# Kernel optimization log

Measured on AMD Instinct MI355X. Metric: run time of the kernel, lower is better.

Reference implementation:

```python
import jax, jax.numpy as jnp
import numpy as np

L, B, P, D, H, DH, KV, M, S, A = 12, 8, 800, 1024, 8, 256, 1, 4096, 50, 32
ROPE_BASE = 10000.0
NEG = -1e30


def _rms(x, w):
    return (x * jax.lax.rsqrt(jnp.mean(x * x, -1, keepdims=True) + 1e-6)) * (1.0 + w)


def _rope(x, cos, sin):
    # x: [B,h,S,DH]; cos/sin: [B,1,S,DH//2]
    x1, x2 = jnp.split(x, 2, axis=-1)
    return jnp.concatenate([x1 * cos - x2 * sin, x2 * cos + x1 * sin], -1)


def setup_inputs() -> dict:
    key = jax.random.key(0)
    ks = iter(jax.random.split(key, 40))
    def nrm(shape, s=0.02):
        return jax.random.normal(next(ks), shape, jnp.float32) * s
    return {
        'prefix_pad_masks': jnp.ones((B, P), jnp.bool_),
        'x_t': jax.random.normal(next(ks), (B, S, A), jnp.float32),
        'timestep': jax.random.uniform(next(ks), (B,), jnp.float32),
        'dt': jnp.full((1,), 0.1, jnp.float32),
        'cache_k': nrm((L, B, KV, P, DH), 1.0),
        'cache_v': nrm((L, B, KV, P, DH), 1.0),
        'w_act_in': nrm((A, D)), 'b_act_in': jnp.zeros((D,), jnp.float32),
        'w_t1': nrm((D, D)), 'b_t1': jnp.zeros((D,), jnp.float32),
        'w_t2': nrm((D, D)), 'b_t2': jnp.zeros((D,), jnp.float32),
        'ln1_w': jnp.zeros((L, D), jnp.float32),
        'ada1_w': nrm((L, D, D)),
        'ln2_w': jnp.zeros((L, D), jnp.float32),
        'wq': nrm((L, D, H * DH)), 'wk': nrm((L, D, KV * DH)),
        'wv': nrm((L, D, KV * DH)), 'wo': nrm((L, H * DH, D)),
        'wg': nrm((L, D, M)), 'wu': nrm((L, D, M)), 'wd': nrm((L, M, D)),
        'lnf_w': jnp.zeros((D,), jnp.float32), 'adaf_w': nrm((D, D)),
        'w_act_out': nrm((D, A)), 'b_act_out': jnp.zeros((A,), jnp.float32),
    }


def reference(prefix_pad_masks, x_t, timestep, dt, cache_k, cache_v,
              w_act_in, b_act_in, w_t1, b_t1, w_t2, b_t2,
              ln1_w, ada1_w, ln2_w, wq, wk, wv, wo, wg, wu, wd,
              lnf_w, adaf_w, w_act_out, b_act_out):
    b, s, _ = x_t.shape
    p = prefix_pad_masks.shape[1]
    # --- embed_suffix: action projection + sinusoidal time -> MLP -> adaRMS cond ---
    suffix = x_t @ w_act_in + b_act_in                              # [B,S,D]
    half = D // 2
    freqs = jnp.exp(-jnp.log(jnp.float32(10000.0)) * jnp.arange(half, dtype=jnp.float32) / half)
    ang = timestep[:, None] * freqs[None, :]
    temb = jnp.concatenate([jnp.sin(ang), jnp.cos(ang)], -1)        # [B,D]
    cond = jax.nn.silu(temb @ w_t1 + b_t1) @ w_t2 + b_t2            # adarms_cond [B,D]
    # --- prefix-suffix 2D attention mask (make_att_2d_masks_trt) ---
    suffix_pad = jnp.ones((b, s), jnp.int32)
    suffix_att = jnp.concatenate([jnp.ones((b, 1), jnp.int32), jnp.zeros((b, s - 1), jnp.int32)], 1)
    cums = jnp.cumsum(suffix_att, 1)
    att2d = cums[:, None, :] <= cums[:, :, None]
    pad2d = (suffix_pad[:, None, :] * suffix_pad[:, :, None]).astype(bool)
    pre2d = jnp.broadcast_to(prefix_pad_masks[:, None, :], (b, s, p))
    full = jnp.concatenate([pre2d, att2d & pad2d], 2)               # [B,S,P+S]
    bias = jnp.where(full, 0.0, NEG)[:, None, :, :].astype(jnp.float32)
    # --- position ids: prefix offset + suffix cumsum - 1 ---
    offs = jnp.sum(prefix_pad_masks.astype(jnp.int32), -1)[:, None]
    pos = offs + jnp.cumsum(suffix_pad, 1) - 1                      # [B,S]
    inv = 1.0 / (ROPE_BASE ** (jnp.arange(0, DH, 2, dtype=jnp.float32) / DH))
    rang = pos[..., None].astype(jnp.float32) * inv                 # [B,S,DH/2]
    cos = jnp.cos(rang)[:, None]
    sin = jnp.sin(rang)[:, None]
    # --- gemma expert (eager attention over KV cache + suffix) ---
    h = suffix * jnp.sqrt(jnp.float32(D))
    def layer(hc, xs):
        l1, a1, l2, Wq, Wk, Wv, Wo, Wg, Wu, Wd, ck, cv = xs
        x = _rms(hc, l1) * (1.0 + (cond @ a1)[:, None, :])
        q = (x @ Wq).reshape(b, s, H, DH).transpose(0, 2, 1, 3)
        k = (x @ Wk).reshape(b, s, KV, DH).transpose(0, 2, 1, 3)
        v = (x @ Wv).reshape(b, s, KV, DH).transpose(0, 2, 1, 3)
        q = _rope(q, cos, sin)
        k = _rope(k, cos, sin)
        kf = jnp.repeat(jnp.concatenate([ck, k], 2), H // KV, 1)    # [B,H,P+S,DH]
        vf = jnp.repeat(jnp.concatenate([cv, v], 2), H // KV, 1)
        sc = jnp.einsum('bhsd,bhtd->bhst', q, kf) / jnp.sqrt(jnp.float32(DH)) + bias
        at = jax.nn.softmax(sc, -1)
        o = jnp.einsum('bhst,bhtd->bhsd', at, vf).transpose(0, 2, 1, 3).reshape(b, s, H * DH)
        hc = hc + o @ Wo
        x2 = _rms(hc, l2)
        hc = hc + (jax.nn.gelu(x2 @ Wg, approximate=True) * (x2 @ Wu)) @ Wd
        return hc, None
    h, _ = jax.lax.scan(layer, h, (ln1_w, ada1_w, ln2_w, wq, wk, wv, wo, wg, wu, wd, cache_k, cache_v))
    hf = _rms(h, lnf_w) * (1.0 + (cond @ adaf_w)[:, None, :])
    v_t = hf[:, -S:].astype(jnp.float32) @ w_act_out + b_act_out    # action_out_proj
    return x_t + dt.reshape(1, 1, 1) * v_t                          # Euler step
```

## Files before the change

### kernel.cpp

```cpp
#include <hip/hip_runtime.h>
#include <hip/hip_bf16.h>
#include <math.h>

#define NLAYER 12
#define NB 8
#define NP 800
#define ND 1024
#define NH 8
#define NDH 256
#define NM 4096
#define NS 50
#define NA 32
#define NKEYS 850
#define KPAD 1024

typedef unsigned short ushort_t;
typedef unsigned int u32;
using f32x4  = __attribute__((ext_vector_type(4))) float;
using short8 = __attribute__((ext_vector_type(8))) short;

__device__ __forceinline__ u32 pack_bf2(float lo, float hi) {
  u32 a = __float_as_uint(lo);
  u32 b = __float_as_uint(hi);
  a += 0x7fffu + ((a >> 16) & 1u);
  b += 0x7fffu + ((b >> 16) & 1u);
  return (a >> 16) | (b & 0xffff0000u);
}
__device__ __forceinline__ ushort_t bf1(float x) {
  u32 a = __float_as_uint(x);
  a += 0x7fffu + ((a >> 16) & 1u);
  return (ushort_t)(a >> 16);
}
__device__ __forceinline__ float ubf(ushort_t h) {
  return __uint_as_float(((u32)h) << 16);
}
__device__ __forceinline__ void async_cp16(const void* g, const void* l) {
  __builtin_amdgcn_global_load_lds(
      (const __attribute__((address_space(1))) u32*)g,
      (__attribute__((address_space(3))) u32*)l, 16, 0, 0);
}
#define SWZ(row, c) ((c) ^ (((row) & 7) << 3))


__global__ void cvt_permute_kernel(const float* __restrict__ src, ushort_t* __restrict__ dst, long nrows) {
  long idx = (long)blockIdx.x * 256 + threadIdx.x;
  long row = idx >> 5;
  int t = (int)(idx & 31);
  if (row >= nrows) return;
  const float* s = src + row * 256 + t * 4;
  float4 lo = *reinterpret_cast<const float4*>(s);
  float4 hi = *reinterpret_cast<const float4*>(s + 128);
  ushort_t* d = dst + row * 256 + t * 8;
  *reinterpret_cast<uint4*>(d) =
      make_uint4(pack_bf2(lo.x, hi.x), pack_bf2(lo.y, hi.y),
                 pack_bf2(lo.z, hi.z), pack_bf2(lo.w, hi.w));
}

template<int MODE>
__global__ __launch_bounds__(256) void transpose_cvt(
    const float* __restrict__ src, long sz, ushort_t* __restrict__ dst, long dz,
    int R, int C, int ldd, int halfOff) {
  __shared__ float Ls[64][65];
  const float* s = src + (long)blockIdx.z * sz;
  ushort_t* d    = dst + (long)blockIdx.z * dz;
  int c0 = blockIdx.x * 64, r0 = blockIdx.y * 64;
  int t = threadIdx.x;
  int rr = t >> 4;
  int cc = (t & 15) * 4;
#pragma unroll
  for (int j = 0; j < 4; ++j) {
    int rl = rr + j * 16;
    int r = r0 + rl;
    float4 v = make_float4(0.f, 0.f, 0.f, 0.f);
    if (r < R) v = *reinterpret_cast<const float4*>(s + (long)r * C + c0 + cc);
    Ls[rl][cc] = v.x; Ls[rl][cc+1] = v.y; Ls[rl][cc+2] = v.z; Ls[rl][cc+3] = v.w;
  }
  __syncthreads();
  int dr = t >> 2;
  int rc = (t & 3) * 16;
  int cg = c0 + dr;
  long orow;
  if (MODE == 0)      orow = cg;
  else if (MODE == 1) orow = ((long)(cg >> 5) << 6) + (cg & 31) + halfOff;
  else                orow = (long)(cg & ~255) + ((cg & 127) << 1) + ((cg >> 7) & 1);
  ushort_t* drow = d + orow * ldd + r0 + rc;
#pragma unroll
  for (int i = 0; i < 16; i += 2) {
    int sr = r0 + rc + i;
    if (sr < R) {
      u32 p = pack_bf2(Ls[rc + i][dr], Ls[rc + i + 1][dr]);
      *reinterpret_cast<u32*>(drow + i) = p;
    }
  }
}


__global__ void temb_kernel(const float* __restrict__ ts, float* __restrict__ temb) {
  int idx = blockIdx.x * 256 + threadIdx.x;
  if (idx >= NB * ND) return;
  int b = idx >> 10, d = idx & 1023;
  int i = d & 511;
  float f = __expf(-logf(10000.f) * (float)i / 512.f);
  float ang = ts[b] * f;
  temb[idx] = (d < 512) ? sinf(ang) : cosf(ang);
}

__global__ void suffix_kernel(const float* __restrict__ x_t, const float* __restrict__ w,
                              const float* __restrict__ bias, float* __restrict__ h) {
  int m = blockIdx.x;
  __shared__ float xs[NA];
  if (threadIdx.x < NA) xs[threadIdx.x] = x_t[m * NA + threadIdx.x];
  __syncthreads();
  for (int n = threadIdx.x; n < ND; n += 256) {
    float acc = bias[n];
#pragma unroll
    for (int k = 0; k < NA; ++k) acc += xs[k] * w[k * ND + n];
    h[m * ND + n] = acc * 32.0f;
  }
}

__global__ void rope_table_kernel(float* __restrict__ cosT, float* __restrict__ sinT) {
  int idx = blockIdx.x * 256 + threadIdx.x;
  if (idx >= NS * 128) return;
  int s = idx >> 7, i = idx & 127;
  float inv = __expf(-(float)(2 * i) / 256.f * logf(10000.f));
  float ang = (float)(NP + s) * inv;
  cosT[idx] = cosf(ang);
  sinT[idx] = sinf(ang);
}

template<bool BFOUT>
__global__ void rms_kernel(float* __restrict__ hin, const float* __restrict__ slabs,
                           const float* __restrict__ w,
                           const float* __restrict__ ada, void* __restrict__ outv) {
  int m = blockIdx.x;
  int b = m / NS;
  int d0 = threadIdx.x * 4;
  float4 v = *reinterpret_cast<const float4*>(hin + (long)m * ND + d0);
  if (slabs) {
#pragma unroll
    for (int c = 0; c < 4; ++c) {
      float4 sv = *reinterpret_cast<const float4*>(slabs + ((long)c * 400 + m) * ND + d0);
      v.x += sv.x; v.y += sv.y; v.z += sv.z; v.w += sv.w;
    }
    *reinterpret_cast<float4*>(hin + (long)m * ND + d0) = v;
  }
  float ss = v.x*v.x + v.y*v.y + v.z*v.z + v.w*v.w;
#pragma unroll
  for (int off = 32; off > 0; off >>= 1) ss += __shfl_down(ss, off);
  __shared__ float red[4];
  int lane = threadIdx.x & 63, wid = threadIdx.x >> 6;
  if (lane == 0) red[wid] = ss;
  __syncthreads();
  float tot = red[0] + red[1] + red[2] + red[3];
  float r = rsqrtf(tot * (1.f / ND) + 1e-6f);
  float4 wv = *reinterpret_cast<const float4*>(w + d0);
  float4 o;
  o.x = v.x * r * (1.f + wv.x);
  o.y = v.y * r * (1.f + wv.y);
  o.z = v.z * r * (1.f + wv.z);
  o.w = v.w * r * (1.f + wv.w);
  if (ada) {
    float4 av = *reinterpret_cast<const float4*>(ada + (long)b * ND + d0);
    o.x *= (1.f + av.x); o.y *= (1.f + av.y); o.z *= (1.f + av.z); o.w *= (1.f + av.w);
  }
  if (BFOUT) {
    *reinterpret_cast<uint2*>((ushort_t*)outv + (long)m * ND + d0) =
        make_uint2(pack_bf2(o.x, o.y), pack_bf2(o.z, o.w));
  } else {
    *reinterpret_cast<float4*>((float*)outv + (long)m * ND + d0) = o;
  }
}

__global__ void final_fused(const float* __restrict__ hin, const float* __restrict__ slabs,
                            const float* __restrict__ lnf,
                            const float* __restrict__ adaf, const float* __restrict__ w,
                            const float* __restrict__ bias, const float* __restrict__ x_t,
                            const float* __restrict__ dt, float* __restrict__ out) {
  int m = blockIdx.x;
  int b = m / NS;
  int d0 = threadIdx.x * 4;
  __shared__ float hfs[ND];
  __shared__ float red[256];
  float4 v = *reinterpret_cast<const float4*>(hin + (long)m * ND + d0);
#pragma unroll
  for (int c = 0; c < 4; ++c) {
    float4 sv = *reinterpret_cast<const float4*>(slabs + ((long)c * 400 + m) * ND + d0);
    v.x += sv.x; v.y += sv.y; v.z += sv.z; v.w += sv.w;
  }
  float ss = v.x*v.x + v.y*v.y + v.z*v.z + v.w*v.w;
#pragma unroll
  for (int off = 32; off > 0; off >>= 1) ss += __shfl_down(ss, off);
  __shared__ float red4[4];
  int lane = threadIdx.x & 63, wid = threadIdx.x >> 6;
  if (lane == 0) red4[wid] = ss;
  __syncthreads();
  float tot = red4[0] + red4[1] + red4[2] + red4[3];
  float r = rsqrtf(tot * (1.f / ND) + 1e-6f);
  float4 wv = *reinterpret_cast<const float4*>(lnf + d0);
  float4 av = *reinterpret_cast<const float4*>(adaf + (long)b * ND + d0);
  hfs[d0]     = v.x * r * (1.f + wv.x) * (1.f + av.x);
  hfs[d0 + 1] = v.y * r * (1.f + wv.y) * (1.f + av.y);
  hfs[d0 + 2] = v.z * r * (1.f + wv.z) * (1.f + av.z);
  hfs[d0 + 3] = v.w * r * (1.f + wv.w) * (1.f + av.w);
  __syncthreads();
  int a = threadIdx.x & 31;
  int kg = threadIdx.x >> 5;
  float acc = 0.f;
  for (int k = kg; k < ND; k += 8) acc += hfs[k] * w[k * NA + a];
  red[threadIdx.x] = acc;
  __syncthreads();
  if (threadIdx.x < NA) {
    float s = 0.f;
#pragma unroll
    for (int g = 0; g < 8; ++g) s += red[g * 32 + a];
    out[m * NA + a] = x_t[m * NA + a] + dt[0] * (s + bias[a]);
  }
}

__global__ __launch_bounds__(256) void gemm64slab(
    const ushort_t* __restrict__ A,
    const ushort_t* __restrict__ B,
    float* __restrict__ C,
    int M, int N, int K, int lda, int ldb, int ldc, int kpb) {
  const int flat3 = blockIdx.x + 7 * (blockIdx.y + 16 * blockIdx.z);
  const int wgid = (flat3 & 7) * 56 + (flat3 >> 3);
  const int chunk = wgid / 112;
  const int rem = wgid - chunk * 112;
  const int m0 = (rem % 7) * 64;
  const int n0 = (rem / 7) * 64;
  const int kbeg = chunk * kpb;
  const int kend = kbeg + kpb;

  const int tid = threadIdx.x;
  const int lane = tid & 63;
  const int wbase = tid & 192;
  const int wid = wbase >> 6;
  const int wm = (wid >> 1) * 32;
  const int wn = (wid & 1) * 32;
  const int l15 = lane & 15;
  const int l4  = lane >> 4;

  __shared__ ushort_t As[2][64 * 64];
  __shared__ ushort_t Bs[2][64 * 64];

  f32x4 acc[2][2] = {};

  const int ci0 = wbase + lane;
  const int row0 = ci0 >> 3;
  const int kc0 = (((ci0 & 7) ^ (row0 & 7)) << 3);
  const int ci1 = 256 + ci0;
  const int row1 = ci1 >> 3;
  const int kc1 = (((ci1 & 7) ^ (row1 & 7)) << 3);
  int gra0 = m0 + row0; if (gra0 > M - 1) gra0 = M - 1;
  int gra1 = m0 + row1; if (gra1 > M - 1) gra1 = M - 1;
  const int n_0 = n0 + row0;
  const int n_1 = n0 + row1;

  auto stage = [&](int buf, int k0) {
    async_cp16(A + (long)gra0 * lda + k0 + kc0, (const char*)As[buf] + ci0 * 16);
    async_cp16(B + (long)n_0 * ldb + k0 + kc0, (const char*)Bs[buf] + ci0 * 16);
    async_cp16(A + (long)gra1 * lda + k0 + kc1, (const char*)As[buf] + ci1 * 16);
    async_cp16(B + (long)n_1 * ldb + k0 + kc1, (const char*)Bs[buf] + ci1 * 16);
  };

  const int nt = (kend - kbeg) >> 6;
  stage(0, kbeg);
  __syncthreads();
  int cur = 0;
  for (int t = 0; t < nt; ++t) {
    if (t + 1 < nt) stage(cur ^ 1, kbeg + (t + 1) * 64);
    const ushort_t* Ac = As[cur];
    const ushort_t* Bc = Bs[cur];
#pragma unroll
    for (int ks = 0; ks < 2; ++ks) {
      short8 af[2], bf[2];
#pragma unroll
      for (int mi = 0; mi < 2; ++mi) {
        int row = wm + mi * 16 + l15;
        af[mi] = *reinterpret_cast<const short8*>(&Ac[row * 64 + SWZ(row, ks * 32 + l4 * 8)]);
      }
#pragma unroll
      for (int ni = 0; ni < 2; ++ni) {
        int row = wn + ni * 16 + l15;
        bf[ni] = *reinterpret_cast<const short8*>(&Bc[row * 64 + SWZ(row, ks * 32 + l4 * 8)]);
      }
#pragma unroll
      for (int mi = 0; mi < 2; ++mi)
#pragma unroll
        for (int ni = 0; ni < 2; ++ni)
          acc[mi][ni] = __builtin_amdgcn_mfma_f32_16x16x32_bf16(af[mi], bf[ni], acc[mi][ni], 0, 0, 0);
    }
    __syncthreads();
    cur ^= 1;
  }

  float* Cs = C + (long)chunk * 400 * ldc;
#pragma unroll
  for (int mi = 0; mi < 2; ++mi) {
#pragma unroll
    for (int ni = 0; ni < 2; ++ni) {
      int col = n0 + wn + ni * 16 + l15;
      int rb  = m0 + wm + mi * 16 + l4 * 4;
      if (col >= N) continue;
#pragma unroll
      for (int r = 0; r < 4; ++r) {
        int row = rb + r;
        if (row >= M) continue;
        Cs[(long)row * ldc + col] = acc[mi][ni][r];
      }
    }
  }
}

__global__ __launch_bounds__(256) void gemm64rope(
    const ushort_t* __restrict__ A,
    const ushort_t* __restrict__ B,
    const float* __restrict__ cosT, const float* __restrict__ sinT,
    ushort_t* __restrict__ qTo, ushort_t* __restrict__ k_new,
    ushort_t* __restrict__ vT_l) {
  const int M = 400, lda = 1024, ldb = 1024;
  const int flat = blockIdx.x + 7 * blockIdx.y;
  const int wgid = (flat & 7) * 35 + (flat >> 3);
  const int m0 = (wgid % 7) * 64;
  const int n0 = (wgid / 7) * 64;
  const int tid = threadIdx.x;
  const int lane = tid & 63;
  const int wbase = tid & 192;
  const int wid = wbase >> 6;
  const int wm = (wid >> 1) * 32;
  const int wn = (wid & 1) * 32;
  const int l15 = lane & 15;
  const int l4  = lane >> 4;

  __shared__ ushort_t As[2][64 * 64];
  __shared__ ushort_t Bs[2][64 * 64];

  f32x4 acc[2][2] = {};

  const int ci0 = wbase + lane;
  const int row0 = ci0 >> 3;
  const int kc0 = (((ci0 & 7) ^ (row0 & 7)) << 3);
  const int ci1 = 256 + ci0;
  const int row1 = ci1 >> 3;
  const int kc1 = (((ci1 & 7) ^ (row1 & 7)) << 3);
  int gra0 = m0 + row0; if (gra0 > M - 1) gra0 = M - 1;
  int gra1 = m0 + row1; if (gra1 > M - 1) gra1 = M - 1;
  const int n_0 = n0 + row0;
  const int n_1 = n0 + row1;

  auto stage = [&](int buf, int k0) {
    async_cp16(A + (long)gra0 * lda + k0 + kc0, (const char*)As[buf] + ci0 * 16);
    async_cp16(B + (long)n_0 * ldb + k0 + kc0, (const char*)Bs[buf] + ci0 * 16);
    async_cp16(A + (long)gra1 * lda + k0 + kc1, (const char*)As[buf] + ci1 * 16);
    async_cp16(B + (long)n_1 * ldb + k0 + kc1, (const char*)Bs[buf] + ci1 * 16);
  };

  stage(0, 0);
  __syncthreads();
  int cur = 0;
  for (int t = 0; t < 16; ++t) {
    if (t + 1 < 16) stage(cur ^ 1, (t + 1) * 64);
    const ushort_t* Ac = As[cur];
    const ushort_t* Bc = Bs[cur];
#pragma unroll
    for (int ks = 0; ks < 2; ++ks) {
      short8 af[2], bf[2];
#pragma unroll
      for (int mi = 0; mi < 2; ++mi) {
        int row = wm + mi * 16 + l15;
        af[mi] = *reinterpret_cast<const short8*>(&Ac[row * 64 + SWZ(row, ks * 32 + l4 * 8)]);
      }
#pragma unroll
      for (int ni = 0; ni < 2; ++ni) {
        int row = wn + ni * 16 + l15;
        bf[ni] = *reinterpret_cast<const short8*>(&Bc[row * 64 + SWZ(row, ks * 32 + l4 * 8)]);
      }
#pragma unroll
      for (int mi = 0; mi < 2; ++mi)
#pragma unroll
        for (int ni = 0; ni < 2; ++ni)
          acc[mi][ni] = __builtin_amdgcn_mfma_f32_16x16x32_bf16(af[mi], bf[ni], acc[mi][ni], 0, 0, 0);
    }
    __syncthreads();
    cur ^= 1;
  }

#pragma unroll
  for (int mi = 0; mi < 2; ++mi) {
#pragma unroll
    for (int ni = 0; ni < 2; ++ni) {
      int col = n0 + wn + ni * 16 + l15;
      int rb  = m0 + wm + mi * 16 + l4 * 4;
      float pv[4];
#pragma unroll
      for (int r = 0; r < 4; ++r) pv[r] = __shfl_xor(acc[mi][ni][r], 1);
#pragma unroll
      for (int r = 0; r < 4; ++r) {
        int row = rb + r;
        if (row >= 400) continue;
        int b = row / NS, s = row - b * NS;
        float v = acc[mi][ni][r];
        if (col < 2304) {
          int j = col & 255;
          int i = j >> 1;
          float c = cosT[s * 128 + i], sn = sinT[s * 128 + i];
          float o = (col & 1) ? (v * c + pv[r] * sn) : (v * c - pv[r] * sn);
          if (col < 2048)
            qTo[((long)((b << 3) + (col >> 8)) * NS + s) * 256 + j] = bf1(o);
          else
            k_new[(long)row * 256 + j] = bf1(o);
        } else {
          vT_l[((long)(b * 256 + (col - 2304))) * KPAD + NP + s] = bf1(v);
        }
      }
    }
  }
}

__global__ __launch_bounds__(256) void flash2_kernel(
    const ushort_t* __restrict__ qT,
    const ushort_t* __restrict__ kcache_l,
    const ushort_t* __restrict__ k_new,
    const ushort_t* __restrict__ vT_l,
    const ushort_t* __restrict__ zpad,
    float* __restrict__ opart, float* __restrict__ mpart, float* __restrict__ lpart) {
  const int flat = blockIdx.x + 64 * blockIdx.y;
  const int wgid = (flat & 7) * 32 + (flat >> 3);
  const int bh = wgid & 63;
  const int ch = wgid >> 6;
  const int b  = bh >> 3;
  const int tid = threadIdx.x;
  const int lane = tid & 63;
  const int w = tid >> 6;
  const int wm = (w >> 1) * 32;
  const int wn = (w & 1) * 128;
  const int l15 = lane & 15;
  const int l4  = lane >> 4;

  __shared__ __align__(16) char lds[100352];
  ushort_t* KV0 = (ushort_t*)lds;
  ushort_t* KV1 = (ushort_t*)(lds + 32768);
  ushort_t* Ps  = (ushort_t*)(lds + 65536);
  float* SMm = (float*)(lds + 99328);
  float* SMl = (float*)(lds + 99840);

  short8 qf[4][2][2];
  {
    const ushort_t* qbase = qT + (long)bh * NS * 256;
#pragma unroll
    for (int mi = 0; mi < 2; ++mi) {
      int row = wm + mi * 16 + l15;
      int qr = row < NS ? row : NS - 1;
      const ushort_t* qrow = qbase + (long)qr * 256;
#pragma unroll
      for (int s = 0; s < 4; ++s)
#pragma unroll
        for (int ks = 0; ks < 2; ++ks)
          qf[s][mi][ks] = *reinterpret_cast<const short8*>(qrow + s * 64 + ks * 32 + l4 * 8);
    }
  }

  auto stageK = [&](ushort_t* buf, int s) {
#pragma unroll
    for (int i = 0; i < 8; ++i) {
      int ci = i * 256 + tid;
      int key = ch * 256 + (ci >> 3);
      int seg = (ci ^ (ci >> 3)) & 7;
      const ushort_t* src;
      if (key < NP)         src = kcache_l + ((long)(b * NP + key)) * 256 + s * 64 + seg * 8;
      else if (key < NKEYS) src = k_new + ((long)(b * NS + key - NP)) * 256 + s * 64 + seg * 8;
      else                  src = zpad + seg * 8;
      async_cp16(src, (char*)buf + ci * 16);
    }
  };
  auto stageV = [&](ushort_t* buf, int s) {
#pragma unroll
    for (int i = 0; i < 8; ++i) {
      int ci = i * 256 + tid;
      int dout = ci >> 3;
      int seg = (ci ^ (ci >> 3)) & 7;
      async_cp16(vT_l + ((long)(b * 256 + dout)) * KPAD + ch * 256 + s * 64 + seg * 8,
                 (char*)buf + ci * 16);
    }
  };

  f32x4 s2[2][8] = {};
  stageK(KV0, 0);
  __syncthreads();
#pragma unroll
  for (int s = 0; s < 4; ++s) {
    ushort_t* buf = (s & 1) ? KV1 : KV0;
    ushort_t* nxt = (s & 1) ? KV0 : KV1;
    if (s < 3) stageK(nxt, s + 1);
    __builtin_amdgcn_s_setprio(1);
#pragma unroll
    for (int ks = 0; ks < 2; ++ks) {
      short8 bf[8];
#pragma unroll
      for (int ni = 0; ni < 8; ++ni) {
        int row = wn + ni * 16 + l15;
        bf[ni] = *reinterpret_cast<const short8*>(&buf[row * 64 + SWZ(row, ks * 32 + l4 * 8)]);
      }
#pragma unroll
      for (int mi = 0; mi < 2; ++mi)
#pragma unroll
        for (int ni = 0; ni < 8; ++ni)
          s2[mi][ni] = __builtin_amdgcn_mfma_f32_16x16x32_bf16(qf[s][mi][ks], bf[ni], s2[mi][ni], 0, 0, 0);
    }
    __builtin_amdgcn_s_setprio(0);
    __syncthreads();
  }

  stageV(KV0, 0);

  float mx[2][4];
#pragma unroll
  for (int mi = 0; mi < 2; ++mi)
#pragma unroll
    for (int r = 0; r < 4; ++r) mx[mi][r] = -1e30f;
#pragma unroll
  for (int mi = 0; mi < 2; ++mi)
#pragma unroll
    for (int ni = 0; ni < 8; ++ni) {
      int key = ch * 256 + wn + ni * 16 + l15;
      bool valid = key < NKEYS;
#pragma unroll
      for (int r = 0; r < 4; ++r) {
        float v = s2[mi][ni][r] * 0.0625f;
        v = valid ? v : -1e30f;
        s2[mi][ni][r] = v;
        mx[mi][r] = fmaxf(mx[mi][r], v);
      }
    }
#pragma unroll
  for (int off = 1; off < 16; off <<= 1)
#pragma unroll
    for (int mi = 0; mi < 2; ++mi)
#pragma unroll
      for (int r = 0; r < 4; ++r)
        mx[mi][r] = fmaxf(mx[mi][r], __shfl_xor(mx[mi][r], off));
  if (l15 == 0) {
#pragma unroll
    for (int mi = 0; mi < 2; ++mi)
#pragma unroll
      for (int r = 0; r < 4; ++r)
        SMm[(w & 1) * 64 + wm + mi * 16 + l4 * 4 + r] = mx[mi][r];
  }
  __syncthreads();
  float mrow[2][4], sum[2][4];
#pragma unroll
  for (int mi = 0; mi < 2; ++mi)
#pragma unroll
    for (int r = 0; r < 4; ++r) {
      int row = wm + mi * 16 + l4 * 4 + r;
      mrow[mi][r] = fmaxf(SMm[row], SMm[64 + row]);
      sum[mi][r] = 0.f;
    }
#pragma unroll
  for (int mi = 0; mi < 2; ++mi)
#pragma unroll
    for (int ni = 0; ni < 8; ++ni) {
      int colp = wn + ni * 16 + l15;
#pragma unroll
      for (int r = 0; r < 4; ++r) {
        float e = __expf(s2[mi][ni][r] - mrow[mi][r]);
        Ps[(wm + mi * 16 + l4 * 4 + r) * 264 + colp] = bf1(e);
        sum[mi][r] += e;
      }
    }
#pragma unroll
  for (int off = 1; off < 16; off <<= 1)
#pragma unroll
    for (int mi = 0; mi < 2; ++mi)
#pragma unroll
      for (int r = 0; r < 4; ++r)
        sum[mi][r] += __shfl_xor(sum[mi][r], off);
  if (l15 == 0) {
#pragma unroll
    for (int mi = 0; mi < 2; ++mi)
#pragma unroll
      for (int r = 0; r < 4; ++r)
        SMl[(w & 1) * 64 + wm + mi * 16 + l4 * 4 + r] = sum[mi][r];
  }
  __syncthreads();
  if ((w & 1) == 0 && l15 == 0) {
#pragma unroll
    for (int mi = 0; mi < 2; ++mi)
#pragma unroll
      for (int r = 0; r < 4; ++r) {
        int row = wm + mi * 16 + l4 * 4 + r;
        if (row < NS) {
          mpart[((long)bh * 4 + ch) * NS + row] = mrow[mi][r];
          lpart[((long)bh * 4 + ch) * NS + row] = SMl[row] + SMl[64 + row];
        }
      }
  }

  f32x4 o2[2][8] = {};
#pragma unroll
  for (int s = 0; s < 4; ++s) {
    ushort_t* buf = (s & 1) ? KV1 : KV0;
    ushort_t* nxt = (s & 1) ? KV0 : KV1;
    if (s < 3) stageV(nxt, s + 1);
    __builtin_amdgcn_s_setprio(1);
#pragma unroll
    for (int ks = 0; ks < 2; ++ks) {
      short8 af[2], bf[8];
#pragma unroll
      for (int mi = 0; mi < 2; ++mi)
        af[mi] = *reinterpret_cast<const short8*>(&Ps[(wm + mi * 16 + l15) * 264 + s * 64 + ks * 32 + l4 * 8]);
#pragma unroll
      for (int ni = 0; ni < 8; ++ni) {
        int row = wn + ni * 16 + l15;
        bf[ni] = *reinterpret_cast<const short8*>(&buf[row * 64 + SWZ(row, ks * 32 + l4 * 8)]);
      }
#pragma unroll
      for (int mi = 0; mi < 2; ++mi)
#pragma unroll
        for (int ni = 0; ni < 8; ++ni)
          o2[mi][ni] = __builtin_amdgcn_mfma_f32_16x16x32_bf16(af[mi], bf[ni], o2[mi][ni], 0, 0, 0);
    }
    __builtin_amdgcn_s_setprio(0);
    __syncthreads();
  }

#pragma unroll
  for (int mi = 0; mi < 2; ++mi)
#pragma unroll
    for (int ni = 0; ni < 8; ++ni) {
      int col = wn + ni * 16 + l15;
#pragma unroll
      for (int r = 0; r < 4; ++r) {
        int row = wm + mi * 16 + l4 * 4 + r;
        if (row < NS)
          opart[(((long)bh * 4 + ch) * NS + row) * 256 + col] = o2[mi][ni][r];
      }
    }
}

__global__ void att_combine(const float* __restrict__ opart, const float* __restrict__ mpart,
                            const float* __restrict__ lpart, ushort_t* __restrict__ o_buf) {
  int blk = blockIdx.x;
  int b = blk / NS, s = blk - b * NS;
  int d = threadIdx.x;
  for (int h = 0; h < NH; ++h) {
    int bh = b * NH + h;
    float mv[4];
    float m = -1e30f;
#pragma unroll
    for (int c = 0; c < 4; ++c) {
      mv[c] = mpart[((long)bh * 4 + c) * NS + s];
      m = fmaxf(m, mv[c]);
    }
    float den = 0.f, o = 0.f;
#pragma unroll
    for (int c = 0; c < 4; ++c) {
      float wgt = __expf(mv[c] - m);
      den += wgt * lpart[((long)bh * 4 + c) * NS + s];
      o   += wgt * opart[(((long)bh * 4 + c) * NS + s) * 256 + d];
    }
    o_buf[(long)blk * 2048 + h * 256 + d] = bf1(o / den);
  }
}

__global__ __launch_bounds__(256) void gemm64G(
    const ushort_t* __restrict__ A, const ushort_t* __restrict__ B,
    ushort_t* __restrict__ C, int M, int K, int lda, int ldb, int ldc) {
  const int flat = blockIdx.x + 7 * blockIdx.y;
  const int wgid = (flat & 7) * 112 + (flat >> 3);
  const int m0 = (wgid % 7) * 64;
  const int n0 = (wgid / 7) * 64;
  const int tid = threadIdx.x;
  const int lane = tid & 63;
  const int wbase = tid & 192;
  const int wid = wbase >> 6;
  const int l15 = lane & 15;
  const int l4  = lane >> 4;

  __shared__ ushort_t As[2][64 * 64];
  __shared__ ushort_t Bs[2][64 * 64];

  f32x4 acc[4] = {};

  const int ci0 = wbase + lane;
  const int row0 = ci0 >> 3;
  const int kc0 = (((ci0 & 7) ^ (row0 & 7)) << 3);
  const int ci1 = 256 + ci0;
  const int row1 = ci1 >> 3;
  const int kc1 = (((ci1 & 7) ^ (row1 & 7)) << 3);
  int gra0 = m0 + row0; if (gra0 > M - 1) gra0 = M - 1;
  int gra1 = m0 + row1; if (gra1 > M - 1) gra1 = M - 1;

  auto stage = [&](int buf, int k0) {
    async_cp16(A + (long)gra0 * lda + k0 + kc0, (const char*)As[buf] + ci0 * 16);
    async_cp16(B + (long)(n0 + row0) * ldb + k0 + kc0, (const char*)Bs[buf] + ci0 * 16);
    async_cp16(A + (long)gra1 * lda + k0 + kc1, (const char*)As[buf] + ci1 * 16);
    async_cp16(B + (long)(n0 + row1) * ldb + k0 + kc1, (const char*)Bs[buf] + ci1 * 16);
  };

  const int nt = K >> 6;
  stage(0, 0);
  __syncthreads();
  int cur = 0;
  for (int t = 0; t < nt; ++t) {
    if (t + 1 < nt) stage(cur ^ 1, (t + 1) * 64);
    const ushort_t* Ac = As[cur];
    const ushort_t* Bc = Bs[cur];
#pragma unroll
    for (int ks = 0; ks < 2; ++ks) {
      int arow = wid * 16 + l15;
      short8 af = *reinterpret_cast<const short8*>(&Ac[arow * 64 + SWZ(arow, ks * 32 + l4 * 8)]);
#pragma unroll
      for (int ni = 0; ni < 4; ++ni) {
        int row = ni * 16 + l15;
        short8 bf = *reinterpret_cast<const short8*>(&Bc[row * 64 + SWZ(row, ks * 32 + l4 * 8)]);
        acc[ni] = __builtin_amdgcn_mfma_f32_16x16x32_bf16(af, bf, acc[ni], 0, 0, 0);
      }
    }
    __syncthreads();
    cur ^= 1;
  }

#pragma unroll
  for (int ni = 0; ni < 2; ++ni) {
    int col = (n0 >> 1) + ni * 16 + l15;
    int rb  = m0 + wid * 16 + l4 * 4;
#pragma unroll
    for (int r = 0; r < 4; ++r) {
      int row = rb + r;
      if (row >= M) continue;
      float g = acc[ni][r];
      float u = acc[ni + 2][r];
      float inner = 0.7978845608028654f * (g + 0.044715f * g * g * g);
      float t = g / (1.f + __expf(-2.f * inner));
      C[(long)row * ldc + col] = bf1(t * u);
    }
  }
}

template<int EPI>
__global__ __launch_bounds__(256)
void gemm_f32_kernel(const float* __restrict__ A,
                     const float* __restrict__ B1,
                     float* __restrict__ C,
                     int M, int N, int K, int lda, int ldb, int ldc,
                     const float* __restrict__ bias) {
  const int m0 = blockIdx.x * 64;
  const int n0 = blockIdx.y * 64;
  const int tid = threadIdx.x;
  const int lane = tid & 63;
  const int wid = tid >> 6;
  const int wm = (wid >> 1) * 32;
  const int wn = (wid & 1) * 32;
  const int l15 = lane & 15;
  const int l4  = lane >> 4;

  __shared__ __align__(16) ushort_t As[64][72];
  __shared__ __align__(16) ushort_t Bs[64][72];

  f32x4 acc[2][2] = {};

  for (int k0 = 0; k0 < K; k0 += 64) {
#pragma unroll
    for (int pass = 0; pass < 2; ++pass) {
      int c = tid + pass * 256;
      int row = c >> 3;
      int kc = (c & 7) * 8;
      int gr = m0 + row, gk = k0 + kc;
      float v[8];
#pragma unroll
      for (int j = 0; j < 8; ++j)
        v[j] = (gr < M && gk + j < K) ? A[(long)gr * lda + gk + j] : 0.f;
      *reinterpret_cast<uint4*>(&As[row][kc]) =
          make_uint4(pack_bf2(v[0],v[1]), pack_bf2(v[2],v[3]),
                     pack_bf2(v[4],v[5]), pack_bf2(v[6],v[7]));
    }
    {
      int n = tid & 63;
      int kg = tid >> 6;
      int gn = n0 + n;
      u32 pk[8];
#pragma unroll
      for (int kk = 0; kk < 16; kk += 2) {
        int kga = k0 + kg * 16 + kk;
        float v0 = (gn < N && kga < K)     ? B1[(long)kga * ldb + gn] : 0.f;
        float v1 = (gn < N && kga + 1 < K) ? B1[(long)(kga + 1) * ldb + gn] : 0.f;
        pk[kk >> 1] = pack_bf2(v0, v1);
      }
      *reinterpret_cast<uint4*>(&Bs[n][kg * 16])     = make_uint4(pk[0],pk[1],pk[2],pk[3]);
      *reinterpret_cast<uint4*>(&Bs[n][kg * 16 + 8]) = make_uint4(pk[4],pk[5],pk[6],pk[7]);
    }
    __syncthreads();
#pragma unroll
    for (int ks = 0; ks < 2; ++ks) {
      short8 af[2], bfr[2];
#pragma unroll
      for (int mi = 0; mi < 2; ++mi)
        af[mi] = *reinterpret_cast<const short8*>(&As[wm + mi*16 + l15][ks*32 + l4*8]);
#pragma unroll
      for (int ni = 0; ni < 2; ++ni)
        bfr[ni] = *reinterpret_cast<const short8*>(&Bs[wn + ni*16 + l15][ks*32 + l4*8]);
#pragma unroll
      for (int mi = 0; mi < 2; ++mi)
#pragma unroll
        for (int ni = 0; ni < 2; ++ni)
          acc[mi][ni] = __builtin_amdgcn_mfma_f32_16x16x32_bf16(af[mi], bfr[ni], acc[mi][ni], 0, 0, 0);
    }
    __syncthreads();
  }

#pragma unroll
  for (int mi = 0; mi < 2; ++mi) {
#pragma unroll
    for (int ni = 0; ni < 2; ++ni) {
      int col = n0 + wn + ni * 16 + l15;
      int rb  = m0 + wm + mi * 16 + l4 * 4;
#pragma unroll
      for (int r = 0; r < 4; ++r) {
        int row = rb + r;
        if (row < M && col < N) {
          float v = acc[mi][ni][r];
          if (EPI == 1) C[(long)row * ldc + col] = v + bias[col];
          else {
            float t = v + bias[col];
            C[(long)row * ldc + col] = t / (1.f + __expf(-t));
          }
        }
      }
    }
  }
}

__global__ __launch_bounds__(256)
void gemm_f32sk(const float* __restrict__ A,
                const float* __restrict__ B, long bz,
                float* __restrict__ C, long cz,
                int M, int N, int K, int lda, int ldb, int ldc, int nks) {
  const int zz = blockIdx.z;
  const int layer = zz / nks;
  const int chunk = zz % nks;
  const int kpb = K / nks;
  const int kbeg = chunk * kpb, kend = kbeg + kpb;
  const float* Bb = B + (long)layer * bz;
  float* Cb = C + (long)layer * cz;

  const int m0 = blockIdx.x * 64;
  const int n0 = blockIdx.y * 64;
  const int tid = threadIdx.x;
  const int lane = tid & 63;
  const int wid = tid >> 6;
  const int wm = (wid >> 1) * 32;
  const int wn = (wid & 1) * 32;
  const int l15 = lane & 15;
  const int l4  = lane >> 4;

  __shared__ __align__(16) ushort_t As[64][72];
  __shared__ __align__(16) ushort_t Bs[64][72];

  f32x4 acc[2][2] = {};

  for (int k0 = kbeg; k0 < kend; k0 += 64) {
#pragma unroll
    for (int pass = 0; pass < 2; ++pass) {
      int c = tid + pass * 256;
      int row = c >> 3;
      int kc = (c & 7) * 8;
      int gr = m0 + row, gk = k0 + kc;
      float v[8];
#pragma unroll
      for (int j = 0; j < 8; ++j)
        v[j] = (gr < M) ? A[(long)gr * lda + gk + j] : 0.f;
      *reinterpret_cast<uint4*>(&As[row][kc]) =
          make_uint4(pack_bf2(v[0],v[1]), pack_bf2(v[2],v[3]),
                     pack_bf2(v[4],v[5]), pack_bf2(v[6],v[7]));
    }
    {
      int n = tid & 63;
      int kg = tid >> 6;
      int gn = n0 + n;
      u32 pk[8];
#pragma unroll
      for (int kk = 0; kk < 16; kk += 2) {
        int kga = k0 + kg * 16 + kk;
        float v0 = Bb[(long)kga * ldb + gn];
        float v1 = Bb[(long)(kga + 1) * ldb + gn];
        pk[kk >> 1] = pack_bf2(v0, v1);
      }
      *reinterpret_cast<uint4*>(&Bs[n][kg * 16])     = make_uint4(pk[0],pk[1],pk[2],pk[3]);
      *reinterpret_cast<uint4*>(&Bs[n][kg * 16 + 8]) = make_uint4(pk[4],pk[5],pk[6],pk[7]);
    }
    __syncthreads();
#pragma unroll
    for (int ks = 0; ks < 2; ++ks) {
      short8 af[2], bfr[2];
#pragma unroll
      for (int mi = 0; mi < 2; ++mi)
        af[mi] = *reinterpret_cast<const short8*>(&As[wm + mi*16 + l15][ks*32 + l4*8]);
#pragma unroll
      for (int ni = 0; ni < 2; ++ni)
        bfr[ni] = *reinterpret_cast<const short8*>(&Bs[wn + ni*16 + l15][ks*32 + l4*8]);
#pragma unroll
      for (int mi = 0; mi < 2; ++mi)
#pragma unroll
        for (int ni = 0; ni < 2; ++ni)
          acc[mi][ni] = __builtin_amdgcn_mfma_f32_16x16x32_bf16(af[mi], bfr[ni], acc[mi][ni], 0, 0, 0);
    }
    __syncthreads();
  }

#pragma unroll
  for (int mi = 0; mi < 2; ++mi) {
#pragma unroll
    for (int ni = 0; ni < 2; ++ni) {
      int col = n0 + wn + ni * 16 + l15;
      int rb  = m0 + wm + mi * 16 + l4 * 4;
#pragma unroll
      for (int r = 0; r < 4; ++r) {
        int row = rb + r;
        if (row < M && col < N)
          atomicAdd(&Cb[(long)row * ldc + col], acc[mi][ni][r]);
      }
    }
  }
}

extern "C" void kernel_launch(void* const* d_in, const int* in_sizes, int n_in,
                              void* d_out, int out_size, void* d_ws, size_t ws_size,
                              hipStream_t stream) {
  (void)in_sizes; (void)n_in; (void)out_size; (void)ws_size;
  const float* x_t      = (const float*)d_in[1];
  const float* tstep    = (const float*)d_in[2];
  const float* dtp      = (const float*)d_in[3];
  const float* cache_k  = (const float*)d_in[4];
  const float* cache_v  = (const float*)d_in[5];
  const float* w_act_in = (const float*)d_in[6];
  const float* b_act_in = (const float*)d_in[7];
  const float* w_t1     = (const float*)d_in[8];
  const float* b_t1     = (const float*)d_in[9];
  const float* w_t2     = (const float*)d_in[10];
  const float* b_t2     = (const float*)d_in[11];
  const float* ln1_w    = (const float*)d_in[12];
  const float* ada1_w   = (const float*)d_in[13];
  const float* ln2_w    = (const float*)d_in[14];
  const float* wq       = (const float*)d_in[15];
  const float* wk       = (const float*)d_in[16];
  const float* wv       = (const float*)d_in[17];
  const float* wo       = (const float*)d_in[18];
  const float* wg       = (const float*)d_in[19];
  const float* wu       = (const float*)d_in[20];
  const float* wd       = (const float*)d_in[21];
  const float* lnf_w    = (const float*)d_in[22];
  const float* adaf_w   = (const float*)d_in[23];
  const float* wao      = (const float*)d_in[24];
  const float* bao      = (const float*)d_in[25];
  float* outp = (float*)d_out;

  char* p = (char*)d_ws;
  auto alloc = [&](size_t bytes) { char* r = p; p += (bytes + 255) & ~(size_t)255; return r; };

  ushort_t* wqkvT  = (ushort_t*)alloc((size_t)12 * 2560 * 1024 * 2);
  ushort_t* woT    = (ushort_t*)alloc((size_t)12 * 1024 * 2048 * 2);
  ushort_t* wguT   = (ushort_t*)alloc((size_t)12 * 8192 * 1024 * 2);
  ushort_t* wdT    = (ushort_t*)alloc((size_t)12 * 1024 * 4096 * 2);
  ushort_t* kcache = (ushort_t*)alloc((size_t)12 * 8 * NP * 256 * 2);
  ushort_t* vT     = (ushort_t*)alloc((size_t)12 * 8 * 256 * KPAD * 2);
  ushort_t* qT     = (ushort_t*)alloc((size_t)64 * NS * 256 * 2);
  ushort_t* k_new  = (ushort_t*)alloc((size_t)400 * 256 * 2);
  float*    opart  = (float*)alloc((size_t)64 * 4 * NS * 256 * 4);
  float*    mpart  = (float*)alloc((size_t)64 * 4 * NS * 4);
  float*    lpart  = (float*)alloc((size_t)64 * 4 * NS * 4);
  float*    woP    = (float*)alloc((size_t)4 * 400 * 1024 * 4);
  float*    wdP    = (float*)alloc((size_t)4 * 400 * 1024 * 4);
  ushort_t* o_buf  = (ushort_t*)alloc((size_t)400 * 2048 * 2);
  ushort_t* t_buf  = (ushort_t*)alloc((size_t)400 * 4096 * 2);
  ushort_t* x_buf  = (ushort_t*)alloc((size_t)400 * 1024 * 2);
  float*    h_buf  = (float*)alloc((size_t)400 * 1024 * 4);
  float*    temb   = (float*)alloc(8 * 1024 * 4);
  float*    tmp    = (float*)alloc(8 * 1024 * 4);
  float*    cond   = (float*)alloc(8 * 1024 * 4);
  float*    ada_all= (float*)alloc((size_t)12 * 8 * 1024 * 4);
  float*    adaf_o = (float*)alloc(8 * 1024 * 4);
  float*    cosT   = (float*)alloc(NS * 128 * 4);
  float*    sinT   = (float*)alloc(NS * 128 * 4);
  ushort_t* zpad   = (ushort_t*)alloc(512 * 2);

  hipMemsetAsync(zpad, 0, 512 * 2, stream);
  hipMemsetAsync(ada_all, 0, ((size_t)12 * 8 * 1024 + 8 * 1024) * 4, stream);

  cvt_permute_kernel<<<9600, 256, 0, stream>>>(cache_k, kcache, (long)12 * 8 * NP);
  transpose_cvt<2><<<dim3(32, 16, 12), 256, 0, stream>>>(wq, (long)1024 * 2048, wqkvT, (long)2560 * 1024, 1024, 2048, 1024, 0);
  transpose_cvt<2><<<dim3(4, 16, 12), 256, 0, stream>>>(wk, (long)1024 * 256, wqkvT + (long)2048 * 1024, (long)2560 * 1024, 1024, 256, 1024, 0);
  transpose_cvt<0><<<dim3(4, 16, 12), 256, 0, stream>>>(wv, (long)1024 * 256, wqkvT + (long)2304 * 1024, (long)2560 * 1024, 1024, 256, 1024, 0);
  transpose_cvt<0><<<dim3(16, 32, 12), 256, 0, stream>>>(wo, (long)2048 * 1024, woT, (long)1024 * 2048, 2048, 1024, 2048, 0);
  transpose_cvt<1><<<dim3(64, 16, 12), 256, 0, stream>>>(wg, (long)1024 * 4096, wguT, (long)8192 * 1024, 1024, 4096, 1024, 0);
  transpose_cvt<1><<<dim3(64, 16, 12), 256, 0, stream>>>(wu, (long)1024 * 4096, wguT, (long)8192 * 1024, 1024, 4096, 1024, 32);
  transpose_cvt<0><<<dim3(16, 64, 12), 256, 0, stream>>>(wd, (long)4096 * 1024, wdT, (long)1024 * 4096, 4096, 1024, 4096, 0);
  transpose_cvt<0><<<dim3(4, 13, 96), 256, 0, stream>>>(cache_v, (long)NP * 256, vT, (long)256 * KPAD, NP, 256, KPAD, 0);

  temb_kernel<<<32, 256, 0, stream>>>(tstep, temb);
  suffix_kernel<<<400, 256, 0, stream>>>(x_t, w_act_in, b_act_in, h_buf);
  rope_table_kernel<<<25, 256, 0, stream>>>(cosT, sinT);
  gemm_f32_kernel<2><<<dim3(1, 16, 1), 256, 0, stream>>>(temb, w_t1, tmp, NB, ND, ND, ND, ND, ND, b_t1);
  gemm_f32_kernel<1><<<dim3(1, 16, 1), 256, 0, stream>>>(tmp, w_t2, cond, NB, ND, ND, ND, ND, ND, b_t2);
  gemm_f32sk<<<dim3(1, 16, 48), 256, 0, stream>>>(cond, ada1_w, (long)ND * ND, ada_all, (long)NB * ND, NB, ND, ND, ND, ND, ND, 4);
  gemm_f32sk<<<dim3(1, 16, 4), 256, 0, stream>>>(cond, adaf_w, 0, adaf_o, 0, NB, ND, ND, ND, ND, ND, 4);

  for (int l = 0; l < NLAYER; ++l) {
    ushort_t* vT_l = vT + (long)l * 8 * 256 * KPAD;
    rms_kernel<true><<<400, 256, 0, stream>>>(
        h_buf, l == 0 ? nullptr : wdP, ln1_w + (long)l * ND, ada_all + (long)l * NB * ND, x_buf);
    gemm64rope<<<dim3(7, 40, 1), 256, 0, stream>>>(
        x_buf, wqkvT + (long)l * 2560 * 1024, cosT, sinT, qT, k_new, vT_l);
    flash2_kernel<<<dim3(64, 4, 1), 256, 0, stream>>>(
        qT, kcache + (long)l * 8 * NP * 256, k_new, vT_l, zpad, opart, mpart, lpart);
    att_combine<<<400, 256, 0, stream>>>(opart, mpart, lpart, o_buf);
    gemm64slab<<<dim3(7, 16, 4), 256, 0, stream>>>(
        o_buf, woT + (long)l * 1024 * 2048, woP, 400, 1024, 2048, 2048, 2048, 1024, 512);
    rms_kernel<true><<<400, 256, 0, stream>>>(
        h_buf, woP, ln2_w + (long)l * ND, nullptr, x_buf);
    gemm64G<<<dim3(7, 128, 1), 256, 0, stream>>>(
        x_buf, wguT + (long)l * 8192 * 1024, t_buf, 400, 1024, 1024, 1024, 4096);
    gemm64slab<<<dim3(7, 16, 4), 256, 0, stream>>>(
        t_buf, wdT + (long)l * 1024 * 4096, wdP, 400, 1024, 4096, 4096, 4096, 1024, 1024);
  }

  final_fused<<<400, 256, 0, stream>>>(h_buf, wdP, lnf_w, adaf_o, wao, bao, x_t, dtp, outp);
}
```

Before: 1.811 ms.

## Split attention into 7 key chunks with bf16 partials, double split-K slabs

Attention now splits keys into 7 chunks of 128 instead of 4 chunks of 256, which gives 448 workgroups and uses less LDS per block for higher occupancy. Partial outputs are stored in bf16 to cut the traffic of writing and combining them, at some cost in precision. The Wo and Wd split-K GEMMs use 8 slabs instead of 4 to launch more workgroups, so the RMS kernels must now sum 8 slabs. KPAD shrinks to 896, which reduces V transpose storage.

```diff
diff --git a/kernel.cpp b/kernel.cpp
--- a/kernel.cpp
+++ b/kernel.cpp
@@ -12,7 +12,8 @@
 #define NS 50
 #define NA 32
 #define NKEYS 850
-#define KPAD 1024
+#define KPAD 896
+#define NCH 7
 
 typedef unsigned short ushort_t;
 typedef unsigned int u32;
@@ -139,7 +140,7 @@
   float4 v = *reinterpret_cast<const float4*>(hin + (long)m * ND + d0);
   if (slabs) {
 #pragma unroll
-    for (int c = 0; c < 4; ++c) {
+    for (int c = 0; c < 8; ++c) {
       float4 sv = *reinterpret_cast<const float4*>(slabs + ((long)c * 400 + m) * ND + d0);
       v.x += sv.x; v.y += sv.y; v.z += sv.z; v.w += sv.w;
     }
@@ -184,7 +185,7 @@
   __shared__ float red[256];
   float4 v = *reinterpret_cast<const float4*>(hin + (long)m * ND + d0);
 #pragma unroll
-  for (int c = 0; c < 4; ++c) {
+  for (int c = 0; c < 8; ++c) {
     float4 sv = *reinterpret_cast<const float4*>(slabs + ((long)c * 400 + m) * ND + d0);
     v.x += sv.x; v.y += sv.y; v.z += sv.z; v.w += sv.w;
   }
@@ -224,7 +225,7 @@
     float* __restrict__ C,
     int M, int N, int K, int lda, int ldb, int ldc, int kpb) {
   const int flat3 = blockIdx.x + 7 * (blockIdx.y + 16 * blockIdx.z);
-  const int wgid = (flat3 & 7) * 56 + (flat3 >> 3);
+  const int wgid = (flat3 & 7) * 112 + (flat3 >> 3);
   const int chunk = wgid / 112;
   const int rem = wgid - chunk * 112;
   const int m0 = (rem % 7) * 64;
@@ -418,15 +419,15 @@
   }
 }
 
-__global__ __launch_bounds__(256) void flash2_kernel(
+__global__ __launch_bounds__(256) void flash3_kernel(
     const ushort_t* __restrict__ qT,
     const ushort_t* __restrict__ kcache_l,
     const ushort_t* __restrict__ k_new,
     const ushort_t* __restrict__ vT_l,
     const ushort_t* __restrict__ zpad,
-    float* __restrict__ opart, float* __restrict__ mpart, float* __restrict__ lpart) {
+    ushort_t* __restrict__ opart, float* __restrict__ mpart, float* __restrict__ lpart) {
   const int flat = blockIdx.x + 64 * blockIdx.y;
-  const int wgid = (flat & 7) * 32 + (flat >> 3);
+  const int wgid = (flat & 7) * 56 + (flat >> 3);
   const int bh = wgid & 63;
   const int ch = wgid >> 6;
   const int b  = bh >> 3;
@@ -434,16 +435,17 @@
   const int lane = tid & 63;
   const int w = tid >> 6;
   const int wm = (w >> 1) * 32;
-  const int wn = (w & 1) * 128;
+  const int wnK = (w & 1) * 64;
+  const int wnV = (w & 1) * 64;
   const int l15 = lane & 15;
   const int l4  = lane >> 4;
 
-  __shared__ __align__(16) char lds[100352];
+  __shared__ __align__(16) char lds[51200];
   ushort_t* KV0 = (ushort_t*)lds;
-  ushort_t* KV1 = (ushort_t*)(lds + 32768);
-  ushort_t* Ps  = (ushort_t*)(lds + 65536);
-  float* SMm = (float*)(lds + 99328);
-  float* SMl = (float*)(lds + 99840);
+  ushort_t* KV1 = (ushort_t*)(lds + 16384);
+  ushort_t* Ps  = (ushort_t*)(lds + 32768);
+  float* SMm = (float*)(lds + 50176);
+  float* SMl = (float*)(lds + 50688);
 
   short8 qf[4][2][2];
   {
@@ -463,9 +465,9 @@
 
   auto stageK = [&](ushort_t* buf, int s) {
 #pragma unroll
-    for (int i = 0; i < 8; ++i) {
+    for (int i = 0; i < 4; ++i) {
       int ci = i * 256 + tid;
-      int key = ch * 256 + (ci >> 3);
+      int key = ch * 128 + (ci >> 3);
       int seg = (ci ^ (ci >> 3)) & 7;
       const ushort_t* src;
       if (key < NP)         src = kcache_l + ((long)(b * NP + key)) * 256 + s * 64 + seg * 8;
@@ -474,18 +476,19 @@
       async_cp16(src, (char*)buf + ci * 16);
     }
   };
-  auto stageV = [&](ushort_t* buf, int s) {
-#pragma unroll
-    for (int i = 0; i < 8; ++i) {
+  auto stageV = [&](ushort_t* buf, int p) {
+    int dh = p >> 1, ks2 = p & 1;
+#pragma unroll
+    for (int i = 0; i < 4; ++i) {
       int ci = i * 256 + tid;
-      int dout = ci >> 3;
+      int dout = dh * 128 + (ci >> 3);
       int seg = (ci ^ (ci >> 3)) & 7;
-      async_cp16(vT_l + ((long)(b * 256 + dout)) * KPAD + ch * 256 + s * 64 + seg * 8,
+      async_cp16(vT_l + ((long)(b * 256 + dout)) * KPAD + ch * 128 + ks2 * 64 + seg * 8,
                  (char*)buf + ci * 16);
     }
   };
 
-  f32x4 s2[2][8] = {};
+  f32x4 s2[2][4] = {};
   stageK(KV0, 0);
   __syncthreads();
 #pragma unroll
@@ -496,16 +499,16 @@
     __builtin_amdgcn_s_setprio(1);
 #pragma unroll
     for (int ks = 0; ks < 2; ++ks) {
-      short8 bf[8];
-#pragma unroll
-      for (int ni = 0; ni < 8; ++ni) {
-        int row = wn + ni * 16 + l15;
+      short8 bf[4];
+#pragma unroll
+      for (int ni = 0; ni < 4; ++ni) {
+        int row = wnK + ni * 16 + l15;
         bf[ni] = *reinterpret_cast<const short8*>(&buf[row * 64 + SWZ(row, ks * 32 + l4 * 8)]);
       }
 #pragma unroll
       for (int mi = 0; mi < 2; ++mi)
 #pragma unroll
-        for (int ni = 0; ni < 8; ++ni)
+        for (int ni = 0; ni < 4; ++ni)
           s2[mi][ni] = __builtin_amdgcn_mfma_f32_16x16x32_bf16(qf[s][mi][ks], bf[ni], s2[mi][ni], 0, 0, 0);
     }
     __builtin_amdgcn_s_setprio(0);
@@ -522,8 +525,8 @@
 #pragma unroll
   for (int mi = 0; mi < 2; ++mi)
 #pragma unroll
-    for (int ni = 0; ni < 8; ++ni) {
-      int key = ch * 256 + wn + ni * 16 + l15;
+    for (int ni = 0; ni < 4; ++ni) {
+      int key = ch * 128 + wnK + ni * 16 + l15;
       bool valid = key < NKEYS;
 #pragma unroll
       for (int r = 0; r < 4; ++r) {
@@ -560,12 +563,12 @@
 #pragma unroll
   for (int mi = 0; mi < 2; ++mi)
 #pragma unroll
-    for (int ni = 0; ni < 8; ++ni) {
-      int colp = wn + ni * 16 + l15;
+    for (int ni = 0; ni < 4; ++ni) {
+      int colp = wnK + ni * 16 + l15;
 #pragma unroll
       for (int r = 0; r < 4; ++r) {
         float e = __expf(s2[mi][ni][r] - mrow[mi][r]);
-        Ps[(wm + mi * 16 + l4 * 4 + r) * 264 + colp] = bf1(e);
+        Ps[(wm + mi * 16 + l4 * 4 + r) * 136 + colp] = bf1(e);
         sum[mi][r] += e;
       }
     }
@@ -591,35 +594,36 @@
       for (int r = 0; r < 4; ++r) {
         int row = wm + mi * 16 + l4 * 4 + r;
         if (row < NS) {
-          mpart[((long)bh * 4 + ch) * NS + row] = mrow[mi][r];
-          lpart[((long)bh * 4 + ch) * NS + row] = SMl[row] + SMl[64 + row];
+          mpart[((long)bh * NCH + ch) * NS + row] = mrow[mi][r];
+          lpart[((long)bh * NCH + ch) * NS + row] = SMl[row] + SMl[64 + row];
         }
       }
   }
 
-  f32x4 o2[2][8] = {};
-#pragma unroll
-  for (int s = 0; s < 4; ++s) {
-    ushort_t* buf = (s & 1) ? KV1 : KV0;
-    ushort_t* nxt = (s & 1) ? KV0 : KV1;
-    if (s < 3) stageV(nxt, s + 1);
+  f32x4 o2[2][2][4] = {};
+#pragma unroll
+  for (int p = 0; p < 4; ++p) {
+    ushort_t* buf = (p & 1) ? KV1 : KV0;
+    ushort_t* nxt = (p & 1) ? KV0 : KV1;
+    if (p < 3) stageV(nxt, p + 1);
+    int dh = p >> 1, ks2 = p & 1;
     __builtin_amdgcn_s_setprio(1);
 #pragma unroll
     for (int ks = 0; ks < 2; ++ks) {
-      short8 af[2], bf[8];
+      short8 af[2], bf[4];
 #pragma unroll
       for (int mi = 0; mi < 2; ++mi)
-        af[mi] = *reinterpret_cast<const short8*>(&Ps[(wm + mi * 16 + l15) * 264 + s * 64 + ks * 32 + l4 * 8]);
-#pragma unroll
-      for (int ni = 0; ni < 8; ++ni) {
-        int row = wn + ni * 16 + l15;
+        af[mi] = *reinterpret_cast<const short8*>(&Ps[(wm + mi * 16 + l15) * 136 + ks2 * 64 + ks * 32 + l4 * 8]);
+#pragma unroll
+      for (int ni = 0; ni < 4; ++ni) {
+        int row = wnV + ni * 16 + l15;
         bf[ni] = *reinterpret_cast<const short8*>(&buf[row * 64 + SWZ(row, ks * 32 + l4 * 8)]);
       }
 #pragma unroll
       for (int mi = 0; mi < 2; ++mi)
 #pragma unroll
-        for (int ni = 0; ni < 8; ++ni)
-          o2[mi][ni] = __builtin_amdgcn_mfma_f32_16x16x32_bf16(af[mi], bf[ni], o2[mi][ni], 0, 0, 0);
+        for (int ni = 0; ni < 4; ++ni)
+          o2[mi][dh][ni] = __builtin_amdgcn_mfma_f32_16x16x32_bf16(af[mi], bf[ni], o2[mi][dh][ni], 0, 0, 0);
     }
     __builtin_amdgcn_s_setprio(0);
     __syncthreads();
@@ -628,37 +632,39 @@
 #pragma unroll
   for (int mi = 0; mi < 2; ++mi)
 #pragma unroll
-    for (int ni = 0; ni < 8; ++ni) {
-      int col = wn + ni * 16 + l15;
-#pragma unroll
-      for (int r = 0; r < 4; ++r) {
-        int row = wm + mi * 16 + l4 * 4 + r;
-        if (row < NS)
-          opart[(((long)bh * 4 + ch) * NS + row) * 256 + col] = o2[mi][ni][r];
-      }
-    }
-}
-
-__global__ void att_combine(const float* __restrict__ opart, const float* __restrict__ mpart,
+    for (int dh = 0; dh < 2; ++dh)
+#pragma unroll
+      for (int ni = 0; ni < 4; ++ni) {
+        int col = dh * 128 + wnV + ni * 16 + l15;
+#pragma unroll
+        for (int r = 0; r < 4; ++r) {
+          int row = wm + mi * 16 + l4 * 4 + r;
+          if (row < NS)
+            opart[(((long)bh * NCH + ch) * NS + row) * 256 + col] = bf1(o2[mi][dh][ni][r]);
+        }
+      }
+}
+
+__global__ void att_combine(const ushort_t* __restrict__ opart, const float* __restrict__ mpart,
                             const float* __restrict__ lpart, ushort_t* __restrict__ o_buf) {
   int blk = blockIdx.x;
   int b = blk / NS, s = blk - b * NS;
   int d = threadIdx.x;
   for (int h = 0; h < NH; ++h) {
     int bh = b * NH + h;
-    float mv[4];
+    float mv[NCH];
     float m = -1e30f;
 #pragma unroll
-    for (int c = 0; c < 4; ++c) {
-      mv[c] = mpart[((long)bh * 4 + c) * NS + s];
+    for (int c = 0; c < NCH; ++c) {
+      mv[c] = mpart[((long)bh * NCH + c) * NS + s];
       m = fmaxf(m, mv[c]);
     }
     float den = 0.f, o = 0.f;
 #pragma unroll
-    for (int c = 0; c < 4; ++c) {
+    for (int c = 0; c < NCH; ++c) {
       float wgt = __expf(mv[c] - m);
-      den += wgt * lpart[((long)bh * 4 + c) * NS + s];
-      o   += wgt * opart[(((long)bh * 4 + c) * NS + s) * 256 + d];
+      den += wgt * lpart[((long)bh * NCH + c) * NS + s];
+      o   += wgt * ubf(opart[(((long)bh * NCH + c) * NS + s) * 256 + d]);
     }
     o_buf[(long)blk * 2048 + h * 256 + d] = bf1(o / den);
   }
@@ -967,11 +973,11 @@
   ushort_t* vT     = (ushort_t*)alloc((size_t)12 * 8 * 256 * KPAD * 2);
   ushort_t* qT     = (ushort_t*)alloc((size_t)64 * NS * 256 * 2);
   ushort_t* k_new  = (ushort_t*)alloc((size_t)400 * 256 * 2);
-  float*    opart  = (float*)alloc((size_t)64 * 4 * NS * 256 * 4);
-  float*    mpart  = (float*)alloc((size_t)64 * 4 * NS * 4);
-  float*    lpart  = (float*)alloc((size_t)64 * 4 * NS * 4);
-  float*    woP    = (float*)alloc((size_t)4 * 400 * 1024 * 4);
-  float*    wdP    = (float*)alloc((size_t)4 * 400 * 1024 * 4);
+  ushort_t* opart  = (ushort_t*)alloc((size_t)64 * NCH * NS * 256 * 2);
+  float*    mpart  = (float*)alloc((size_t)64 * NCH * NS * 4);
+  float*    lpart  = (float*)alloc((size_t)64 * NCH * NS * 4);
+  float*    woP    = (float*)alloc((size_t)8 * 400 * 1024 * 4);
+  float*    wdP    = (float*)alloc((size_t)8 * 400 * 1024 * 4);
   ushort_t* o_buf  = (ushort_t*)alloc((size_t)400 * 2048 * 2);
   ushort_t* t_buf  = (ushort_t*)alloc((size_t)400 * 4096 * 2);
   ushort_t* x_buf  = (ushort_t*)alloc((size_t)400 * 1024 * 2);
@@ -1012,17 +1018,17 @@
         h_buf, l == 0 ? nullptr : wdP, ln1_w + (long)l * ND, ada_all + (long)l * NB * ND, x_buf);
     gemm64rope<<<dim3(7, 40, 1), 256, 0, stream>>>(
         x_buf, wqkvT + (long)l * 2560 * 1024, cosT, sinT, qT, k_new, vT_l);
-    flash2_kernel<<<dim3(64, 4, 1), 256, 0, stream>>>(
+    flash3_kernel<<<dim3(64, NCH, 1), 256, 0, stream>>>(
         qT, kcache + (long)l * 8 * NP * 256, k_new, vT_l, zpad, opart, mpart, lpart);
     att_combine<<<400, 256, 0, stream>>>(opart, mpart, lpart, o_buf);
-    gemm64slab<<<dim3(7, 16, 4), 256, 0, stream>>>(
-        o_buf, woT + (long)l * 1024 * 2048, woP, 400, 1024, 2048, 2048, 2048, 1024, 512);
+    gemm64slab<<<dim3(7, 16, 8), 256, 0, stream>>>(
+        o_buf, woT + (long)l * 1024 * 2048, woP, 400, 1024, 2048, 2048, 2048, 1024, 256);
     rms_kernel<true><<<400, 256, 0, stream>>>(
         h_buf, woP, ln2_w + (long)l * ND, nullptr, x_buf);
     gemm64G<<<dim3(7, 128, 1), 256, 0, stream>>>(
         x_buf, wguT + (long)l * 8192 * 1024, t_buf, 400, 1024, 1024, 1024, 4096);
-    gemm64slab<<<dim3(7, 16, 4), 256, 0, stream>>>(
-        t_buf, wdT + (long)l * 1024 * 4096, wdP, 400, 1024, 4096, 4096, 4096, 1024, 1024);
+    gemm64slab<<<dim3(7, 16, 8), 256, 0, stream>>>(
+        t_buf, wdT + (long)l * 1024 * 4096, wdP, 400, 1024, 4096, 4096, 4096, 1024, 512);
   }
 
   final_fused<<<400, 256, 0, stream>>>(h_buf, wdP, lnf_w, adaf_o, wao, bao, x_t, dtp, outp);
```

Measured after the change: 1.769 ms (median of 2 runs). 1.02x faster.
